# Optimization experiments

Measured on AMD Instinct MI355X. Metric: run time of the kernel, lower is better.

Reference implementation:

```python
import jax, jax.numpy as jnp
import numpy as np

N, IN_CHN, MDIM, ATT_D, NUM_CLS = 100000, 1024, 512, 128, 2
NUM_GROUP, INST_PER_GROUP = 8, 4
GROUP_SIZE = N // NUM_GROUP


def setup_inputs() -> dict:
    key = jax.random.key(0)
    ks = jax.random.split(key, 8)
    def w(k, shape, fan):
        return (jax.random.normal(k, shape, jnp.float32) / np.sqrt(fan)).astype(jnp.float32)
    return {
        "index_chunk_list": jax.random.randint(ks[0], (NUM_GROUP, GROUP_SIZE), 0, N),
        "tfeat_tensor": jax.random.normal(ks[1], (N, IN_CHN), jnp.float32),
        # DimReduction: Linear(1024 -> mDim) + ReLU (numLayer_Res = 0)
        "W1": w(ks[2], (MDIM, IN_CHN), IN_CHN), "b1": jnp.zeros((MDIM,), jnp.float32),
        # Attention: Linear(mDim -> 128), tanh, Linear(128 -> 1)
        "Wa1": w(ks[3], (ATT_D, MDIM), MDIM), "ba1": jnp.zeros((ATT_D,), jnp.float32),
        "Wa2": w(ks[4], (1, ATT_D), ATT_D), "ba2": jnp.zeros((1,), jnp.float32),
        # Classifier_1fc: Linear(mDim -> num_cls)  (dropout=0 -> identity)
        "Wc": w(ks[5], (NUM_CLS, MDIM), MDIM), "bc": jnp.zeros((NUM_CLS,), jnp.float32),
    }


def _group_forward(idx, tfeat, W1, b1, Wa1, ba1, Wa2, ba2, Wc, bc):
    # idx: [S] instance indices for one pseudo-bag
    sub = jnp.take(tfeat, idx, axis=0)                       # [S, in_chn]  gather
    mid = jax.nn.relu(sub @ W1.T + b1)                       # [S, m]       DimReduction
    a = jnp.tanh(mid @ Wa1.T + ba1) @ Wa2.T + ba2            # [S, 1]       Attention logits
    a = jax.nn.softmax(a[:, 0], axis=0)                      # [S]          softmax over instances
    att = mid * a[:, None]                                   # [S, m]       einsum('ns,n->ns')
    bag = att.sum(axis=0)                                    # [m]          attention-weighted sum
    pred = bag @ Wc.T + bc                                    # [C]          bag-level logits
    # get_cam_1d: per-instance logits from classifier weight only (no bias)
    cam = jax.nn.softmax(att @ Wc.T, axis=1)                  # [S, C]
    order = jnp.argsort(-cam[:, -1])                          # descending sort on last-class prob
    topk = jnp.concatenate([order[:INST_PER_GROUP], order[-INST_PER_GROUP:]])
    maxmin = jnp.take(mid, topk, axis=0)                      # [2k, m]  MaxMinS distill feats
    return pred, maxmin


def reference(index_chunk_list, tfeat_tensor, W1, b1, Wa1, ba1, Wa2, ba2, Wc, bc):
    f = jax.vmap(_group_forward, in_axes=(0,) + (None,) * 9)
    slide_sub_preds, slide_pseudo_feat = f(index_chunk_list, tfeat_tensor,
                                           W1, b1, Wa1, ba1, Wa2, ba2, Wc, bc)
    # [numGroup, num_cls], [numGroup, 2*instance_per_group, mDim]
    return slide_sub_preds, slide_pseudo_feat
```

## Files before the change

kernel.cpp:

```cpp
#include <hip/hip_runtime.h>
#include <stdint.h>

#define N_TOT 100000
#define IN_CHN 1024
#define MDIM 512
#define ATT_D 128
#define NUM_GROUP 8
#define GROUP_SIZE 12500
#define SEGB 196

typedef __bf16 bf16x8 __attribute__((ext_vector_type(8)));
typedef float f32x4 __attribute__((ext_vector_type(4)));
typedef unsigned short u16x8 __attribute__((ext_vector_type(8)));

__device__ __forceinline__ unsigned short f2bf(float x){
  union { float f; unsigned u; } v; v.f = x;
  unsigned r = v.u + 0x7fffu + ((v.u >> 16) & 1u);
  return (unsigned short)(r >> 16);
}
__device__ __forceinline__ float bf2f(unsigned short h){
  union { unsigned u; float f; } v; v.u = ((unsigned)h) << 16; return v.f;
}
__device__ __forceinline__ void gload16(const void* g, void* l){
  __builtin_amdgcn_global_load_lds(
      (const __attribute__((address_space(1))) unsigned int*)g,
      (__attribute__((address_space(3))) unsigned int*)l, 16, 0, 0);
}

__global__ __launch_bounds__(256) void kconv(const float* __restrict__ W1,
                                             const float* __restrict__ Wa1,
                                             unsigned short* __restrict__ W1b,
                                             unsigned short* __restrict__ Wa1b){
  int i = blockIdx.x * 256 + threadIdx.x;
  if (i < MDIM * IN_CHN) W1b[i] = f2bf(W1[i]);
  else {
    int j = i - MDIM * IN_CHN;
    if (j < ATT_D * MDIM) Wa1b[j] = f2bf(Wa1[j]);
  }
}

__global__ __launch_bounds__(512) void kgemm_mid(const int* __restrict__ idxf,
                                                 const float* __restrict__ tfeat,
                                                 const unsigned short* __restrict__ W1b,
                                                 const float* __restrict__ b1,
                                                 const float* __restrict__ Wc,
                                                 unsigned short* __restrict__ midb,
                                                 float* __restrict__ tvp){
  __shared__ alignas(16) float Af[128 * 32];
  __shared__ alignas(16) unsigned short Bs[256 * 32];
  __shared__ int gsm[128];
  __shared__ float dcol[256];
  __shared__ float tvacc[128][4];
  int tid = threadIdx.x;
  int xcd = blockIdx.x & 7, idx = blockIdx.x >> 3;
  int tile = (xcd < 4 ? xcd * 196 : 4 * 196 + (xcd - 4) * 195) + idx;
  int bn = tile & 1, bm = tile >> 1;
  int m0 = bm * 128, n0 = bn * 256;
  if (tid < 128){ int r = m0 + tid; gsm[tid] = idxf[r < N_TOT ? r : 0]; }
  if (tid >= 128 && tid < 384){
    int c = tid - 128;
    dcol[c] = Wc[512 + n0 + c] - Wc[n0 + c];
  }
  __syncthreads();

  int w = tid >> 6, l = tid & 63;
  int l16 = tid & 15, hi = (tid >> 4) & 3;
  int wm = w >> 2, wn = w & 3;

  const float* asrc[2]; int adst[2];
  #pragma unroll
  for (int q = 0; q < 2; q++){
    int rowl = q * 64 + w * 8 + (l >> 3);
    asrc[q] = tfeat + (size_t)gsm[rowl] * IN_CHN + (((l & 7) ^ (l >> 3)) << 2);
    adst[q] = (q * 64 + w * 8) * 32;
  }
  const unsigned short* bsrc[2]; int bdst[2];
  #pragma unroll
  for (int q = 0; q < 2; q++){
    int rowl = q * 128 + w * 16 + (l >> 2);
    bsrc[q] = W1b + (size_t)(n0 + rowl) * IN_CHN + (((l & 3) ^ ((l >> 3) & 3)) << 3);
    bdst[q] = (q * 128 + w * 16) * 32;
  }

  f32x4 acc[4][4];
  #pragma unroll
  for (int a = 0; a < 4; a++)
    #pragma unroll
    for (int b = 0; b < 4; b++) acc[a][b] = (f32x4){0.f, 0.f, 0.f, 0.f};

  int r7 = l16 & 7;
  int b3 = (l16 >> 1) & 3;

  for (int s = 0; s < 32; s++){
    __syncthreads();
    #pragma unroll
    for (int q = 0; q < 2; q++){
      gload16(asrc[q] + s * 32, &Af[adst[q]]);
      gload16(bsrc[q] + s * 32, &Bs[bdst[q]]);
    }
    __syncthreads();

    bf16x8 af[4], bfr[4];
    #pragma unroll
    for (int a = 0; a < 4; a++){
      int row = wm * 64 + a * 16 + l16;
      f32x4 lo  = *(const f32x4*)&Af[row * 32 + (((2 * hi) ^ r7) << 2)];
      f32x4 hi4 = *(const f32x4*)&Af[row * 32 + (((2 * hi + 1) ^ r7) << 2)];
      bf16x8 pk;
      pk[0] = (__bf16)lo[0]; pk[1] = (__bf16)lo[1]; pk[2] = (__bf16)lo[2]; pk[3] = (__bf16)lo[3];
      pk[4] = (__bf16)hi4[0]; pk[5] = (__bf16)hi4[1]; pk[6] = (__bf16)hi4[2]; pk[7] = (__bf16)hi4[3];
      af[a] = pk;
    }
    #pragma unroll
    for (int b = 0; b < 4; b++){
      int row = wn * 64 + b * 16 + l16;
      bfr[b] = *(const bf16x8*)&Bs[row * 32 + ((hi ^ b3) << 3)];
    }
    #pragma unroll
    for (int a = 0; a < 4; a++)
      #pragma unroll
      for (int b = 0; b < 4; b++)
        acc[a][b] = __builtin_amdgcn_mfma_f32_16x16x32_bf16(af[a], bfr[b], acc[a][b], 0, 0, 0);
  }

  float biasv[4];
  #pragma unroll
  for (int b = 0; b < 4; b++) biasv[b] = b1[n0 + wn * 64 + b * 16 + l16];
  #pragma unroll
  for (int a = 0; a < 4; a++){
    #pragma unroll
    for (int q = 0; q < 4; q++){
      int row = m0 + wm * 64 + a * 16 + hi * 4 + q;
      float t = 0.f;
      #pragma unroll
      for (int b = 0; b < 4; b++){
        int colL = wn * 64 + b * 16 + l16;
        float v = fmaxf(acc[a][b][q] + biasv[b], 0.f);
        t += v * dcol[colL];
        if (row < N_TOT) midb[(size_t)row * MDIM + n0 + colL] = f2bf(v);
      }
      t += __shfl_xor(t, 1); t += __shfl_xor(t, 2);
      t += __shfl_xor(t, 4); t += __shfl_xor(t, 8);
      if (l16 == 0) tvacc[wm * 64 + a * 16 + hi * 4 + q][wn] = t;
    }
  }
  __syncthreads();
  if (tid < 128){
    int row = m0 + tid;
    if (row < N_TOT)
      tvp[(size_t)bn * N_TOT + row] = tvacc[tid][0] + tvacc[tid][1] + tvacc[tid][2] + tvacc[tid][3];
  }
}

__global__ __launch_bounds__(256) void kattn(const unsigned short* __restrict__ midb,
                                             const unsigned short* __restrict__ Wa1b,
                                             const float* __restrict__ ba1,
                                             const float* __restrict__ Wa2,
                                             const float* __restrict__ ba2,
                                             float* __restrict__ lv){
  __shared__ alignas(16) unsigned short Asm[128 * 64];
  __shared__ alignas(16) unsigned short Bsm[128 * 64];
  __shared__ float part[128][2];
  int tid = threadIdx.x;
  int m0 = blockIdx.x * 128;

  int w = tid >> 6, l = tid & 63;
  int l16 = tid & 15, hi = (tid >> 4) & 3;
  int wm = tid >> 7, wn = (tid >> 6) & 1;
  int scw = (l & 7) ^ (l >> 3);

  const unsigned short *asrc[4], *bsrc[4];
  int dsto[4];
  #pragma unroll
  for (int q = 0; q < 4; q++){
    int rowl = q * 32 + w * 8 + (l >> 3);
    asrc[q] = midb + (size_t)(m0 + rowl) * MDIM + scw * 8;
    bsrc[q] = Wa1b + (size_t)rowl * MDIM + scw * 8;
    dsto[q] = (q * 32 + w * 8) * 64;
  }

  f32x4 acc[4][4];
  #pragma unroll
  for (int a = 0; a < 4; a++)
    #pragma unroll
    for (int b = 0; b < 4; b++) acc[a][b] = (f32x4){0.f, 0.f, 0.f, 0.f};
  int r7 = l16 & 7;

  for (int s = 0; s < 8; s++){
    __syncthreads();
    #pragma unroll
    for (int q = 0; q < 4; q++){
      gload16(asrc[q] + s * 64, &Asm[dsto[q]]);
      gload16(bsrc[q] + s * 64, &Bsm[dsto[q]]);
    }
    __syncthreads();
    #pragma unroll
    for (int ks = 0; ks < 2; ks++){
      bf16x8 af[4], bfr[4];
      #pragma unroll
      for (int a = 0; a < 4; a++){
        int row = wm * 64 + a * 16 + l16;
        af[a] = *(const bf16x8*)&Asm[row * 64 + (((ks * 4 + hi) ^ r7) << 3)];
      }
      #pragma unroll
      for (int b = 0; b < 4; b++){
        int row = wn * 64 + b * 16 + l16;
        bfr[b] = *(const bf16x8*)&Bsm[row * 64 + (((ks * 4 + hi) ^ r7) << 3)];
      }
      #pragma unroll
      for (int a = 0; a < 4; a++)
        #pragma unroll
        for (int b = 0; b < 4; b++)
          acc[a][b] = __builtin_amdgcn_mfma_f32_16x16x32_bf16(af[a], bfr[b], acc[a][b], 0, 0, 0);
    }
  }
  #pragma unroll
  for (int a = 0; a < 4; a++){
    #pragma unroll
    for (int q = 0; q < 4; q++){
      float v = 0.f;
      #pragma unroll
      for (int b = 0; b < 4; b++){
        int col = wn * 64 + b * 16 + l16;
        v += tanhf(acc[a][b][q] + ba1[col]) * Wa2[col];
      }
      #pragma unroll
      for (int off = 1; off < 16; off <<= 1) v += __shfl_xor(v, off);
      if (l16 == 0) part[wm * 64 + a * 16 + hi * 4 + q][wn] = v;
    }
  }
  __syncthreads();
  if (tid < 128){
    int row = m0 + tid;
    if (row < N_TOT) lv[row] = part[tid][0] + part[tid][1] + ba2[0];
  }
}

__global__ __launch_bounds__(256) void kselect(const float* __restrict__ lv,
                                               const float* __restrict__ tvp,
                                               float* __restrict__ maxlw, float* __restrict__ Zw,
                                               int* __restrict__ cand,
                                               float* __restrict__ w){
  __shared__ float keys[GROUP_SIZE];
  __shared__ float candk[4096];
  __shared__ int   candi[4096];
  __shared__ float rk[256];
  __shared__ int ri[256];
  __shared__ int rs[256];
  __shared__ float sbc;
  int g = blockIdx.x, tid = threadIdx.x;
  const float* lg = lv + (size_t)g * GROUP_SIZE;

  float mx = -1e30f;
  for (int i = tid; i < GROUP_SIZE; i += 256) mx = fmaxf(mx, lg[i]);
  rk[tid] = mx; __syncthreads();
  for (int s = 128; s > 0; s >>= 1){ if (tid < s) rk[tid] = fmaxf(rk[tid], rk[tid + s]); __syncthreads(); }
  if (tid == 0) sbc = rk[0];
  __syncthreads();
  float maxl = sbc;

  float z = 0.f;
  for (int i = tid; i < GROUP_SIZE; i += 256){
    float ez = expf(lg[i] - maxl);
    z += ez;
    size_t gi = (size_t)g * GROUP_SIZE + i;
    keys[i] = ez * (tvp[gi] + tvp[N_TOT + gi]);
  }
  rk[tid] = z; __syncthreads();
  for (int s = 128; s > 0; s >>= 1){ if (tid < s) rk[tid] += rk[tid + s]; __syncthreads(); }
  if (tid == 0){ maxlw[g] = maxl; Zw[g] = rk[0]; }
  __syncthreads();
  float invZ = 1.0f / rk[0];
  for (int i = tid; i < GROUP_SIZE; i += 256)
    w[(size_t)g * GROUP_SIZE + i] = expf(lg[i] - maxl) * invZ;
  __syncthreads();

  {
    float tk[16]; int tix[16];
    #pragma unroll
    for (int j = 0; j < 16; j++){ tk[j] = -1e30f; tix[j] = 0x7fffffff; }
    for (int i = tid; i < GROUP_SIZE; i += 256){
      float ck = keys[i];
      if (ck > tk[15]){
        int ci = i;
        #pragma unroll
        for (int j = 0; j < 16; j++){
          bool ins = ck > tk[j];
          float nk = ins ? ck : tk[j]; int ni = ins ? ci : tix[j];
          float ok = ins ? tk[j] : ck; int oi = ins ? tix[j] : ci;
          tk[j] = nk; tix[j] = ni; ck = ok; ci = oi;
        }
      }
    }
    #pragma unroll
    for (int j = 0; j < 16; j++){ candk[tid * 16 + j] = tk[j]; candi[tid * 16 + j] = tix[j]; }
  }
  __syncthreads();
  for (int it = 0; it < 16; it++){
    float bk = -1e30f; int bi = 0x7fffffff; int bs = -1;
    for (int jj = tid; jj < 4096; jj += 256){
      float k = candk[jj]; int ix = candi[jj];
      if (k > bk || (k == bk && ix < bi)){ bk = k; bi = ix; bs = jj; }
    }
    rk[tid] = bk; ri[tid] = bi; rs[tid] = bs; __syncthreads();
    for (int s = 128; s > 0; s >>= 1){
      if (tid < s){
        if (rk[tid + s] > rk[tid] || (rk[tid + s] == rk[tid] && ri[tid + s] < ri[tid])){
          rk[tid] = rk[tid + s]; ri[tid] = ri[tid + s]; rs[tid] = rs[tid + s];
        }
      }
      __syncthreads();
    }
    if (tid == 0){ cand[g * 32 + it] = ri[0]; candk[rs[0]] = -1e30f; }
    __syncthreads();
  }

  {
    float tk[16]; int tix[16];
    #pragma unroll
    for (int j = 0; j < 16; j++){ tk[j] = 1e30f; tix[j] = -1; }
    for (int i = tid; i < GROUP_SIZE; i += 256){
      float ck = keys[i];
      if (ck <= tk[15]){
        int ci = i;
        #pragma unroll
        for (int j = 0; j < 16; j++){
          bool ins = ck <= tk[j];
          float nk = ins ? ck : tk[j]; int ni = ins ? ci : tix[j];
          float ok = ins ? tk[j] : ck; int oi = ins ? tix[j] : ci;
          tk[j] = nk; tix[j] = ni; ck = ok; ci = oi;
        }
      }
    }
    #pragma unroll
    for (int j = 0; j < 16; j++){ candk[tid * 16 + j] = tk[j]; candi[tid * 16 + j] = tix[j]; }
  }
  __syncthreads();
  for (int it = 0; it < 16; it++){
    float bk = 1e30f; int bi = -1; int bs = -1;
    for (int jj = tid; jj < 4096; jj += 256){
      float k = candk[jj]; int ix = candi[jj];
      if (k < bk || (k == bk && ix > bi)){ bk = k; bi = ix; bs = jj; }
    }
    rk[tid] = bk; ri[tid] = bi; rs[tid] = bs; __syncthreads();
    for (int s = 128; s > 0; s >>= 1){
      if (tid < s){
        if (rk[tid + s] < rk[tid] || (rk[tid + s] == rk[tid] && ri[tid + s] > ri[tid])){
          rk[tid] = rk[tid + s]; ri[tid] = ri[tid + s]; rs[tid] = rs[tid + s];
        }
      }
      __syncthreads();
    }
    if (tid == 0){ cand[g * 32 + 16 + it] = ri[0]; candk[rs[0]] = 1e30f; }
    __syncthreads();
  }
}

__global__ __launch_bounds__(256) void kexact(const int* __restrict__ idxf,
                                              const float* __restrict__ tfeat,
                                              const float* __restrict__ W1,
                                              const float* __restrict__ b1,
                                              const float* __restrict__ Wa1,
                                              const float* __restrict__ ba1,
                                              const float* __restrict__ Wa2,
                                              const float* __restrict__ ba2,
                                              const float* __restrict__ Wc,
                                              const int* __restrict__ cand,
                                              const float* __restrict__ maxlw,
                                              float* __restrict__ emid, float* __restrict__ ekey){
  __shared__ float subs[1024];
  __shared__ float midc[512];
  __shared__ float hs[128];
  __shared__ float red[256];
  __shared__ float tsh;
  int bid = blockIdx.x; int g = bid >> 5, c = bid & 31; int tid = threadIdx.x;
  int s = cand[g * 32 + c];
  int inst = idxf[g * GROUP_SIZE + s];
  ((float4*)subs)[tid] = ((const float4*)(tfeat + (size_t)inst * IN_CHN))[tid];
  __syncthreads();

  float a0 = b1[tid], a1 = b1[tid + 256];
  const float4* w0 = (const float4*)(W1 + (size_t)tid * IN_CHN);
  const float4* w1 = (const float4*)(W1 + ((size_t)tid + 256) * IN_CHN);
  const float4* s4 = (const float4*)subs;
  #pragma unroll 4
  for (int k = 0; k < 256; k++){
    float4 sv = s4[k], wva = w0[k], wvb = w1[k];
    a0 += sv.x * wva.x + sv.y * wva.y + sv.z * wva.z + sv.w * wva.w;
    a1 += sv.x * wvb.x + sv.y * wvb.y + sv.z * wvb.z + sv.w * wvb.w;
  }
  a0 = fmaxf(a0, 0.f); a1 = fmaxf(a1, 0.f);
  midc[tid] = a0; midc[tid + 256] = a1;
  size_t eo = (size_t)(g * 32 + c) * MDIM;
  emid[eo + tid] = a0; emid[eo + tid + 256] = a1;
  __syncthreads();

  if (tid < 128){
    const float4* wr = (const float4*)(Wa1 + (size_t)tid * MDIM);
    const float4* m4 = (const float4*)midc;
    float h = ba1[tid];
    #pragma unroll 4
    for (int j = 0; j < 128; j++){
      float4 mv = m4[j], wv = wr[j];
      h += mv.x * wv.x + mv.y * wv.y + mv.z * wv.z + mv.w * wv.w;
    }
    hs[tid] = tanhf(h) * Wa2[tid];
  }
  __syncthreads();

  float tp = midc[tid] * (Wc[512 + tid] - Wc[tid]) + midc[tid + 256] * (Wc[768 + tid] - Wc[256 + tid]);
  red[tid] = tp; __syncthreads();
  for (int st = 128; st > 0; st >>= 1){ if (tid < st) red[tid] += red[tid + st]; __syncthreads(); }
  if (tid == 0) tsh = red[0];
  __syncthreads();
  red[tid] = (tid < 128) ? hs[tid] : 0.f; __syncthreads();
  for (int st = 128; st > 0; st >>= 1){ if (tid < st) red[tid] += red[tid + st]; __syncthreads(); }
  if (tid == 0){
    float lval = red[0] + ba2[0];
    ekey[g * 32 + c] = expf(lval - maxlw[g]) * tsh;
  }
}

__global__ __launch_bounds__(256) void kbag(const unsigned short* __restrict__ midb,
                                            const float* __restrict__ w,
                                            float* __restrict__ bagp){
  __shared__ float wl[SEGB];
  __shared__ float red[4][512];
  int g = blockIdx.x >> 6, seg = blockIdx.x & 63, tid = threadIdx.x;
  int rg = tid >> 6, lane = tid & 63;
  int i0 = seg * SEGB;
  int nr = GROUP_SIZE - i0; if (nr > SEGB) nr = SEGB;
  size_t base = (size_t)g * GROUP_SIZE;
  if (tid < nr) wl[tid] = w[base + i0 + tid];
  __syncthreads();
  float a[8] = {0.f,0.f,0.f,0.f,0.f,0.f,0.f,0.f};
  const unsigned short* mp = midb + (base + i0) * MDIM + lane * 8;
  for (int i = rg; i < nr; i += 4){
    float wi = wl[i];
    u16x8 v = *(const u16x8*)(mp + (size_t)i * MDIM);
    #pragma unroll
    for (int e = 0; e < 8; e++) a[e] += wi * bf2f((unsigned short)v[e]);
  }
  #pragma unroll
  for (int e = 0; e < 8; e++) red[rg][lane * 8 + e] = a[e];
  __syncthreads();
  if (rg == 0){
    float* dst = bagp + (size_t)blockIdx.x * MDIM + lane * 8;
    #pragma unroll
    for (int e = 0; e < 8; e++){
      int c = lane * 8 + e;
      dst[e] = red[0][c] + red[1][c] + red[2][c] + red[3][c];
    }
  }
}

__global__ __launch_bounds__(256) void kfinal(const float* __restrict__ bagp,
                                              const float* __restrict__ Wc,
                                              const float* __restrict__ bc,
                                              const float* __restrict__ emid,
                                              const float* __restrict__ ekey,
                                              const int* __restrict__ cand,
                                              float* __restrict__ out){
  __shared__ float k32[32];
  __shared__ int s32[32];
  __shared__ int ordv[32];
  __shared__ float r0[256], r1[256];
  int g = blockIdx.x, tid = threadIdx.x;
  if (tid < 32){ k32[tid] = ekey[g * 32 + tid]; s32[tid] = cand[g * 32 + tid]; }
  __syncthreads();
  if (tid == 0){
    unsigned used = 0;
    for (int a = 0; a < 32; a++){
      int best = -1;
      for (int b = 0; b < 32; b++){
        if ((used >> b) & 1u) continue;
        if (best < 0 || k32[b] > k32[best] || (k32[b] == k32[best] && s32[b] < s32[best])) best = b;
      }
      used |= 1u << best;
      ordv[a] = best;
    }
  }
  float p0 = 0.f, p1 = 0.f;
  for (int j = tid; j < 512; j += 256){
    float bv = 0.f;
    for (int s2 = 0; s2 < 64; s2++) bv += bagp[(size_t)(g * 64 + s2) * MDIM + j];
    p0 += bv * Wc[j];
    p1 += bv * Wc[512 + j];
  }
  r0[tid] = p0; r1[tid] = p1; __syncthreads();
  for (int s = 128; s > 0; s >>= 1){ if (tid < s){ r0[tid] += r0[tid + s]; r1[tid] += r1[tid + s]; } __syncthreads(); }
  if (tid == 0){
    out[g * 2 + 0] = r0[0] + bc[0];
    out[g * 2 + 1] = r1[0] + bc[1];
  }
  __syncthreads();
  for (int p = 0; p < 8; p++){
    int cc = ordv[p < 4 ? p : 24 + p];
    const float* src = emid + (size_t)(g * 32 + cc) * MDIM;
    float* dst = out + 16 + (size_t)(g * 8 + p) * MDIM;
    for (int j = tid; j < 512; j += 256) dst[j] = src[j];
  }
}

extern "C" void kernel_launch(void* const* d_in, const int* in_sizes, int n_in,
                              void* d_out, int out_size, void* d_ws, size_t ws_size,
                              hipStream_t stream){
  const int*   idxf = (const int*)d_in[0];
  const float* tfeat= (const float*)d_in[1];
  const float* W1   = (const float*)d_in[2];
  const float* b1   = (const float*)d_in[3];
  const float* Wa1  = (const float*)d_in[4];
  const float* ba1  = (const float*)d_in[5];
  const float* Wa2  = (const float*)d_in[6];
  const float* ba2  = (const float*)d_in[7];
  const float* Wc   = (const float*)d_in[8];
  const float* bc   = (const float*)d_in[9];
  float* out = (float*)d_out;
  (void)in_sizes; (void)n_in; (void)out_size; (void)ws_size;

  char* ws = (char*)d_ws;
  size_t off = 0;
  auto alloc = [&](size_t bytes){ void* p = ws + off; off += (bytes + 255) & ~(size_t)255; return p; };
  float* lv    = (float*)alloc((size_t)N_TOT * 4);
  float* tvp   = (float*)alloc((size_t)2 * N_TOT * 4);
  float* maxlw = (float*)alloc(NUM_GROUP * 4);
  float* Zw    = (float*)alloc(NUM_GROUP * 4);
  int*   cand  = (int*)alloc(NUM_GROUP * 32 * 4);
  float* ekey  = (float*)alloc(NUM_GROUP * 32 * 4);
  float* emid  = (float*)alloc((size_t)NUM_GROUP * 32 * MDIM * 4);
  float* bagp  = (float*)alloc((size_t)NUM_GROUP * 64 * MDIM * 4);
  unsigned short* W1b  = (unsigned short*)alloc((size_t)MDIM * IN_CHN * 2);
  unsigned short* Wa1b = (unsigned short*)alloc((size_t)ATT_D * MDIM * 2);
  unsigned short* midb = (unsigned short*)alloc((size_t)N_TOT * MDIM * 2);
  float* w = tvp;

  kconv<<<2304, 256, 0, stream>>>(W1, Wa1, W1b, Wa1b);
  kgemm_mid<<<1564, 512, 0, stream>>>(idxf, tfeat, W1b, b1, Wc, midb, tvp);
  kattn<<<782, 256, 0, stream>>>(midb, Wa1b, ba1, Wa2, ba2, lv);
  kselect<<<8, 256, 0, stream>>>(lv, tvp, maxlw, Zw, cand, w);
  kexact<<<256, 256, 0, stream>>>(idxf, tfeat, W1, b1, Wa1, ba1, Wa2, ba2, Wc, cand, maxlw, emid, ekey);
  kbag<<<512, 256, 0, stream>>>(midb, w, bagp);
  kfinal<<<8, 256, 0, stream>>>(bagp, Wc, bc, emid, ekey, cand, out);
}
```

Before: 622.5 us.

## Split per-group top/bottom candidate selection across 64 blocks with a merge kernel

The single-block-per-group selection kernel (8 blocks total) is split into three kernels. A stats kernel computes the softmax max, normaliser and weights. A partitioned selection kernel has 64 blocks each find the top-16 and bottom-16 keys in a 1563-element segment using wave shuffles. A small merge kernel then reduces the 128 per-group candidates to the final 32. The aim is to spread the serial selection across more CUs and shorten its reduction chains, at the cost of two extra launches and a separate softmax-weight buffer instead of aliasing tvp.

```diff
diff --git a/kernel.cpp b/kernel.cpp
--- a/kernel.cpp
+++ b/kernel.cpp
@@ -8,6 +8,7 @@
 #define NUM_GROUP 8
 #define GROUP_SIZE 12500
 #define SEGB 196
+#define PSEG 1563
 
 typedef __bf16 bf16x8 __attribute__((ext_vector_type(8)));
 typedef float f32x4 __attribute__((ext_vector_type(4)));
@@ -236,21 +237,13 @@
   }
 }
 
-__global__ __launch_bounds__(256) void kselect(const float* __restrict__ lv,
-                                               const float* __restrict__ tvp,
-                                               float* __restrict__ maxlw, float* __restrict__ Zw,
-                                               int* __restrict__ cand,
-                                               float* __restrict__ w){
-  __shared__ float keys[GROUP_SIZE];
-  __shared__ float candk[4096];
-  __shared__ int   candi[4096];
+__global__ __launch_bounds__(256) void kstat(const float* __restrict__ lv,
+                                             float* __restrict__ maxlw, float* __restrict__ Zw,
+                                             float* __restrict__ w){
   __shared__ float rk[256];
-  __shared__ int ri[256];
-  __shared__ int rs[256];
   __shared__ float sbc;
   int g = blockIdx.x, tid = threadIdx.x;
   const float* lg = lv + (size_t)g * GROUP_SIZE;
-
   float mx = -1e30f;
   for (int i = tid; i < GROUP_SIZE; i += 256) mx = fmaxf(mx, lg[i]);
   rk[tid] = mx; __syncthreads();
@@ -258,14 +251,8 @@
   if (tid == 0) sbc = rk[0];
   __syncthreads();
   float maxl = sbc;
-
   float z = 0.f;
-  for (int i = tid; i < GROUP_SIZE; i += 256){
-    float ez = expf(lg[i] - maxl);
-    z += ez;
-    size_t gi = (size_t)g * GROUP_SIZE + i;
-    keys[i] = ez * (tvp[gi] + tvp[N_TOT + gi]);
-  }
+  for (int i = tid; i < GROUP_SIZE; i += 256) z += expf(lg[i] - maxl);
   rk[tid] = z; __syncthreads();
   for (int s = 128; s > 0; s >>= 1){ if (tid < s) rk[tid] += rk[tid + s]; __syncthreads(); }
   if (tid == 0){ maxlw[g] = maxl; Zw[g] = rk[0]; }
@@ -273,85 +260,139 @@
   float invZ = 1.0f / rk[0];
   for (int i = tid; i < GROUP_SIZE; i += 256)
     w[(size_t)g * GROUP_SIZE + i] = expf(lg[i] - maxl) * invZ;
-  __syncthreads();
-
-  {
-    float tk[16]; int tix[16];
-    #pragma unroll
-    for (int j = 0; j < 16; j++){ tk[j] = -1e30f; tix[j] = 0x7fffffff; }
-    for (int i = tid; i < GROUP_SIZE; i += 256){
-      float ck = keys[i];
-      if (ck > tk[15]){
-        int ci = i;
-        #pragma unroll
-        for (int j = 0; j < 16; j++){
-          bool ins = ck > tk[j];
-          float nk = ins ? ck : tk[j]; int ni = ins ? ci : tix[j];
-          float ok = ins ? tk[j] : ck; int oi = ins ? tix[j] : ci;
-          tk[j] = nk; tix[j] = ni; ck = ok; ci = oi;
-        }
-      }
-    }
-    #pragma unroll
-    for (int j = 0; j < 16; j++){ candk[tid * 16 + j] = tk[j]; candi[tid * 16 + j] = tix[j]; }
+}
+
+__global__ __launch_bounds__(256) void kpsel(const float* __restrict__ w,
+                                             const float* __restrict__ tvp,
+                                             float* __restrict__ ptk, int* __restrict__ pti,
+                                             float* __restrict__ pbk, int* __restrict__ pbi){
+  __shared__ float keys[PSEG];
+  __shared__ float rk[256];
+  __shared__ int rj[256];
+  __shared__ int pslot[16];
+  __shared__ float pvalk[16];
+  int bid = blockIdx.x, tid = threadIdx.x;
+  int g = bid >> 3, p = bid & 7;
+  int i0 = p * PSEG;
+  int nr = GROUP_SIZE - i0; if (nr > PSEG) nr = PSEG;
+  size_t base = (size_t)g * GROUP_SIZE;
+  for (int j = tid; j < nr; j += 256){
+    size_t gi = base + i0 + j;
+    keys[j] = w[gi] * (tvp[gi] + tvp[N_TOT + gi]);
   }
   __syncthreads();
   for (int it = 0; it < 16; it++){
-    float bk = -1e30f; int bi = 0x7fffffff; int bs = -1;
-    for (int jj = tid; jj < 4096; jj += 256){
-      float k = candk[jj]; int ix = candi[jj];
-      if (k > bk || (k == bk && ix < bi)){ bk = k; bi = ix; bs = jj; }
-    }
-    rk[tid] = bk; ri[tid] = bi; rs[tid] = bs; __syncthreads();
-    for (int s = 128; s > 0; s >>= 1){
-      if (tid < s){
-        if (rk[tid + s] > rk[tid] || (rk[tid + s] == rk[tid] && ri[tid + s] < ri[tid])){
-          rk[tid] = rk[tid + s]; ri[tid] = ri[tid + s]; rs[tid] = rs[tid + s];
-        }
-      }
-      __syncthreads();
-    }
-    if (tid == 0){ cand[g * 32 + it] = ri[0]; candk[rs[0]] = -1e30f; }
-    __syncthreads();
-  }
-
-  {
-    float tk[16]; int tix[16];
-    #pragma unroll
-    for (int j = 0; j < 16; j++){ tk[j] = 1e30f; tix[j] = -1; }
-    for (int i = tid; i < GROUP_SIZE; i += 256){
-      float ck = keys[i];
-      if (ck <= tk[15]){
-        int ci = i;
-        #pragma unroll
-        for (int j = 0; j < 16; j++){
-          bool ins = ck <= tk[j];
-          float nk = ins ? ck : tk[j]; int ni = ins ? ci : tix[j];
-          float ok = ins ? tk[j] : ck; int oi = ins ? tix[j] : ci;
-          tk[j] = nk; tix[j] = ni; ck = ok; ci = oi;
-        }
-      }
-    }
-    #pragma unroll
-    for (int j = 0; j < 16; j++){ candk[tid * 16 + j] = tk[j]; candi[tid * 16 + j] = tix[j]; }
-  }
+    float bk = -1e30f; int bj = 0x7fffffff;
+    for (int j = tid; j < nr; j += 256){
+      float k = keys[j];
+      if (k > bk || (k == bk && j < bj)){ bk = k; bj = j; }
+    }
+    rk[tid] = bk; rj[tid] = bj;
+    __syncthreads();
+    if (tid < 64){
+      float k = rk[tid]; int j = rj[tid];
+      #pragma unroll
+      for (int o = 64; o < 256; o += 64){
+        float ko = rk[tid + o]; int jo = rj[tid + o];
+        if (ko > k || (ko == k && jo < j)){ k = ko; j = jo; }
+      }
+      #pragma unroll
+      for (int off = 32; off > 0; off >>= 1){
+        float ko = __shfl_xor(k, off); int jo = __shfl_xor(j, off);
+        if (ko > k || (ko == k && jo < j)){ k = ko; j = jo; }
+      }
+      if (tid == 0){
+        ptk[bid * 16 + it] = k; pti[bid * 16 + it] = i0 + j;
+        pslot[it] = j; pvalk[it] = k;
+        keys[j] = -1e30f;
+      }
+    }
+    __syncthreads();
+  }
+  if (tid < 16) keys[pslot[tid]] = pvalk[tid];
   __syncthreads();
   for (int it = 0; it < 16; it++){
-    float bk = 1e30f; int bi = -1; int bs = -1;
-    for (int jj = tid; jj < 4096; jj += 256){
-      float k = candk[jj]; int ix = candi[jj];
-      if (k < bk || (k == bk && ix > bi)){ bk = k; bi = ix; bs = jj; }
-    }
-    rk[tid] = bk; ri[tid] = bi; rs[tid] = bs; __syncthreads();
-    for (int s = 128; s > 0; s >>= 1){
-      if (tid < s){
-        if (rk[tid + s] < rk[tid] || (rk[tid + s] == rk[tid] && ri[tid + s] > ri[tid])){
-          rk[tid] = rk[tid + s]; ri[tid] = ri[tid + s]; rs[tid] = rs[tid + s];
-        }
-      }
-      __syncthreads();
-    }
-    if (tid == 0){ cand[g * 32 + 16 + it] = ri[0]; candk[rs[0]] = 1e30f; }
+    float bk = 1e30f; int bj = -1;
+    for (int j = tid; j < nr; j += 256){
+      float k = keys[j];
+      if (k < bk || (k == bk && j > bj)){ bk = k; bj = j; }
+    }
+    rk[tid] = bk; rj[tid] = bj;
+    __syncthreads();
+    if (tid < 64){
+      float k = rk[tid]; int j = rj[tid];
+      #pragma unroll
+      for (int o = 64; o < 256; o += 64){
+        float ko = rk[tid + o]; int jo = rj[tid + o];
+        if (ko < k || (ko == k && jo > j)){ k = ko; j = jo; }
+      }
+      #pragma unroll
+      for (int off = 32; off > 0; off >>= 1){
+        float ko = __shfl_xor(k, off); int jo = __shfl_xor(j, off);
+        if (ko < k || (ko == k && jo > j)){ k = ko; j = jo; }
+      }
+      if (tid == 0){
+        pbk[bid * 16 + it] = k; pbi[bid * 16 + it] = i0 + j;
+        keys[j] = 1e30f;
+      }
+    }
+    __syncthreads();
+  }
+}
+
+__global__ __launch_bounds__(256) void kmerge(const float* __restrict__ ptk, const int* __restrict__ pti,
+                                              const float* __restrict__ pbk, const int* __restrict__ pbi,
+                                              int* __restrict__ cand){
+  __shared__ float ck[128];
+  __shared__ int ci[128];
+  __shared__ float rk[256];
+  __shared__ int ri[256];
+  __shared__ int rs[256];
+  int g = blockIdx.x, tid = threadIdx.x;
+  if (tid < 128){ ck[tid] = ptk[g * 128 + tid]; ci[tid] = pti[g * 128 + tid]; }
+  __syncthreads();
+  for (int it = 0; it < 16; it++){
+    float bk = (tid < 128) ? ck[tid] : -1e30f;
+    int bi = (tid < 128) ? ci[tid] : 0x7fffffff;
+    rk[tid] = bk; ri[tid] = bi; rs[tid] = tid;
+    __syncthreads();
+    if (tid < 64){
+      float k = rk[tid]; int ii = ri[tid], ss = rs[tid];
+      #pragma unroll
+      for (int o = 64; o < 256; o += 64){
+        float ko = rk[tid + o]; int io = ri[tid + o]; int so = rs[tid + o];
+        if (ko > k || (ko == k && io < ii)){ k = ko; ii = io; ss = so; }
+      }
+      #pragma unroll
+      for (int off = 32; off > 0; off >>= 1){
+        float ko = __shfl_xor(k, off); int io = __shfl_xor(ii, off); int so = __shfl_xor(ss, off);
+        if (ko > k || (ko == k && io < ii)){ k = ko; ii = io; ss = so; }
+      }
+      if (tid == 0){ cand[g * 32 + it] = ii; ck[ss] = -1e30f; }
+    }
+    __syncthreads();
+  }
+  if (tid < 128){ ck[tid] = pbk[g * 128 + tid]; ci[tid] = pbi[g * 128 + tid]; }
+  __syncthreads();
+  for (int it = 0; it < 16; it++){
+    float bk = (tid < 128) ? ck[tid] : 1e30f;
+    int bi = (tid < 128) ? ci[tid] : -1;
+    rk[tid] = bk; ri[tid] = bi; rs[tid] = tid;
+    __syncthreads();
+    if (tid < 64){
+      float k = rk[tid]; int ii = ri[tid], ss = rs[tid];
+      #pragma unroll
+      for (int o = 64; o < 256; o += 64){
+        float ko = rk[tid + o]; int io = ri[tid + o]; int so = rs[tid + o];
+        if (ko < k || (ko == k && io > ii)){ k = ko; ii = io; ss = so; }
+      }
+      #pragma unroll
+      for (int off = 32; off > 0; off >>= 1){
+        float ko = __shfl_xor(k, off); int io = __shfl_xor(ii, off); int so = __shfl_xor(ss, off);
+        if (ko < k || (ko == k && io > ii)){ k = ko; ii = io; ss = so; }
+      }
+      if (tid == 0){ cand[g * 32 + 16 + it] = ii; ck[ss] = 1e30f; }
+    }
     __syncthreads();
   }
 }
@@ -523,22 +564,28 @@
   auto alloc = [&](size_t bytes){ void* p = ws + off; off += (bytes + 255) & ~(size_t)255; return p; };
   float* lv    = (float*)alloc((size_t)N_TOT * 4);
   float* tvp   = (float*)alloc((size_t)2 * N_TOT * 4);
+  float* wsm   = (float*)alloc((size_t)N_TOT * 4);
   float* maxlw = (float*)alloc(NUM_GROUP * 4);
   float* Zw    = (float*)alloc(NUM_GROUP * 4);
   int*   cand  = (int*)alloc(NUM_GROUP * 32 * 4);
   float* ekey  = (float*)alloc(NUM_GROUP * 32 * 4);
+  float* ptk   = (float*)alloc(64 * 16 * 4);
+  int*   pti   = (int*)alloc(64 * 16 * 4);
+  float* pbk   = (float*)alloc(64 * 16 * 4);
+  int*   pbi   = (int*)alloc(64 * 16 * 4);
   float* emid  = (float*)alloc((size_t)NUM_GROUP * 32 * MDIM * 4);
   float* bagp  = (float*)alloc((size_t)NUM_GROUP * 64 * MDIM * 4);
   unsigned short* W1b  = (unsigned short*)alloc((size_t)MDIM * IN_CHN * 2);
   unsigned short* Wa1b = (unsigned short*)alloc((size_t)ATT_D * MDIM * 2);
   unsigned short* midb = (unsigned short*)alloc((size_t)N_TOT * MDIM * 2);
-  float* w = tvp;
 
   kconv<<<2304, 256, 0, stream>>>(W1, Wa1, W1b, Wa1b);
   kgemm_mid<<<1564, 512, 0, stream>>>(idxf, tfeat, W1b, b1, Wc, midb, tvp);
   kattn<<<782, 256, 0, stream>>>(midb, Wa1b, ba1, Wa2, ba2, lv);
-  kselect<<<8, 256, 0, stream>>>(lv, tvp, maxlw, Zw, cand, w);
+  kstat<<<8, 256, 0, stream>>>(lv, maxlw, Zw, wsm);
+  kpsel<<<64, 256, 0, stream>>>(wsm, tvp, ptk, pti, pbk, pbi);
+  kmerge<<<8, 256, 0, stream>>>(ptk, pti, pbk, pbi, cand);
   kexact<<<256, 256, 0, stream>>>(idxf, tfeat, W1, b1, Wa1, ba1, Wa2, ba2, Wc, cand, maxlw, emid, ekey);
-  kbag<<<512, 256, 0, stream>>>(midb, w, bagp);
+  kbag<<<512, 256, 0, stream>>>(midb, wsm, bagp);
   kfinal<<<8, 256, 0, stream>>>(bagp, Wc, bc, emid, ekey, cand, out);
 }
```

After: 572.4 us. 1.09x faster.
